# Optimization experiments

Measured on AMD Instinct MI355X. Metric: run time of the kernel, lower is better.

## Reference

```python
import jax, jax.numpy as jnp
import numpy as np

TEMPERATURE = 0.5


def setup_inputs() -> dict:
    key = jax.random.key(0)
    k1, k2 = jax.random.split(key)
    B, D = 4096, 256
    z_i = jax.random.normal(k1, (B, D), dtype=jnp.float32)
    z_j = jax.random.normal(k2, (B, D), dtype=jnp.float32)
    return {"z_i": z_i, "z_j": z_j}


def reference(z_i, z_j):
    B = z_i.shape[0]
    N = 2 * B
    z = jnp.concatenate([z_i, z_j], axis=0)                      # [N, D]
    # cosine similarity = normalized dot products (fused: normalize + matmul)
    zn = z / jnp.linalg.norm(z, axis=-1, keepdims=True)
    sim = jnp.einsum('nd,md->nm', zn, zn) / TEMPERATURE          # [N, N]
    # positives: sim[i, i+B] and sim[i+B, i]
    idx = jnp.arange(B)
    pos = jnp.concatenate([sim[idx, idx + B], sim[idx + B, idx]])  # [N]
    # cross-entropy with label 0 over logits [pos, negatives]:
    # logsumexp over row excluding only the diagonal (positive counted once)
    neg_inf = jnp.asarray(-jnp.inf, sim.dtype)
    sim_masked = jnp.where(jnp.eye(N, dtype=bool), neg_inf, sim)
    lse = jax.nn.logsumexp(sim_masked, axis=1)                    # [N]
    loss = jnp.sum(lse - pos) / N
    return loss
```

## Files before the change

kernel.cpp:

```cpp
#include <hip/hip_runtime.h>

typedef __attribute__((ext_vector_type(4))) float f32x4;
typedef __attribute__((ext_vector_type(2))) long long i64x2;

static constexpr int D = 256;
static constexpr float INV_T = 2.0f;
static constexpr float KEXP2 = 2.8853900817779268f;
static constexpr int TTILE = 64;
static constexpr int NT = TTILE * (TTILE + 1) / 2;
static constexpr int NPLANE = 2 * TTILE;
static constexpr int LSE_BLOCKS = 256;

__device__ inline float fexp2(float x) {
#if __has_builtin(__builtin_amdgcn_exp2f)
    return __builtin_amdgcn_exp2f(x);
#else
    return exp2f(x);
#endif
}
__device__ inline unsigned int cvt4_fp8(float a, float b, float c, float d) {
    int v = __builtin_amdgcn_cvt_pk_fp8_f32(a, b, 0, false);
    v = __builtin_amdgcn_cvt_pk_fp8_f32(c, d, v, true);
    return (unsigned int)v;
}

__global__ void k_norm(const float* __restrict__ zi, const float* __restrict__ zj,
                       unsigned char* __restrict__ zn, float* __restrict__ diag,
                       float* __restrict__ pos_partial, unsigned int* __restrict__ counter,
                       int B) {
    __shared__ float red[4];
    const int lane = threadIdx.x & 63;
    const int wv = threadIdx.x >> 6;
    const int i = blockIdx.x * 4 + wv;
    if (blockIdx.x == 0 && threadIdx.x == 0) *counter = 0;
    if (i < B) {
        float4 vi = reinterpret_cast<const float4*>(zi + (size_t)i * D)[lane];
        float4 vj = reinterpret_cast<const float4*>(zj + (size_t)i * D)[lane];
        float ssi = vi.x * vi.x + vi.y * vi.y + vi.z * vi.z + vi.w * vi.w;
        float ssj = vj.x * vj.x + vj.y * vj.y + vj.z * vj.z + vj.w * vj.w;
#pragma unroll
        for (int off = 32; off >= 1; off >>= 1) {
            ssi += __shfl_xor(ssi, off, 64);
            ssj += __shfl_xor(ssj, off, 64);
        }
        float rni = rsqrtf(ssi), rnj = rsqrtf(ssj);
        unsigned int pa = cvt4_fp8(vi.x * rni, vi.y * rni, vi.z * rni, vi.w * rni);
        unsigned int pb = cvt4_fp8(vj.x * rnj, vj.y * rnj, vj.z * rnj, vj.w * rnj);
        float fa0 = __builtin_amdgcn_cvt_f32_fp8((int)pa, 0);
        float fa1 = __builtin_amdgcn_cvt_f32_fp8((int)pa, 1);
        float fa2 = __builtin_amdgcn_cvt_f32_fp8((int)pa, 2);
        float fa3 = __builtin_amdgcn_cvt_f32_fp8((int)pa, 3);
        float fb0 = __builtin_amdgcn_cvt_f32_fp8((int)pb, 0);
        float fb1 = __builtin_amdgcn_cvt_f32_fp8((int)pb, 1);
        float fb2 = __builtin_amdgcn_cvt_f32_fp8((int)pb, 2);
        float fb3 = __builtin_amdgcn_cvt_f32_fp8((int)pb, 3);
        float sdi = fa0 * fa0 + fa1 * fa1 + fa2 * fa2 + fa3 * fa3;
        float sdj = fb0 * fb0 + fb1 * fb1 + fb2 * fb2 + fb3 * fb3;
        float pd  = fa0 * fb0 + fa1 * fb1 + fa2 * fb2 + fa3 * fb3;
#pragma unroll
        for (int off = 32; off >= 1; off >>= 1) {
            sdi += __shfl_xor(sdi, off, 64);
            sdj += __shfl_xor(sdj, off, 64);
            pd  += __shfl_xor(pd, off, 64);
        }
        unsigned int qa = __shfl_xor(pa, 1, 64);
        unsigned int qb = __shfl_xor(pb, 1, 64);
        if ((lane & 1) == 0) {
            int m = lane >> 1;
            size_t base = (size_t)(m >> 3) * 1024 + (size_t)((m & 3) * 16) * 16
                        + (size_t)(((m >> 2) & 1)) * 8;
            size_t offA = (size_t)(i >> 4) * 4096 + base + (size_t)(i & 15) * 16;
            int ib = i + B;
            size_t offB = (size_t)(ib >> 4) * 4096 + base + (size_t)(ib & 15) * 16;
            *reinterpret_cast<unsigned long long*>(zn + offA) =
                ((unsigned long long)qa << 32) | pa;
            *reinterpret_cast<unsigned long long*>(zn + offB) =
                ((unsigned long long)qb << 32) | pb;
        }
        if (lane == 0) {
            diag[i]     = -fexp2(KEXP2 * sdi);
            diag[i + B] = -fexp2(KEXP2 * sdj);
            red[wv] = pd;
        }
    } else if (lane == 0) {
        red[wv] = 0.f;
    }
    __syncthreads();
    if (threadIdx.x == 0)
        pos_partial[blockIdx.x] = 2.0f * INV_T * (red[0] + red[1] + red[2] + red[3]);
}

__global__ __launch_bounds__(128, 2)
void k_main(const unsigned char* __restrict__ zn, float* __restrict__ P, int N) {
    const int tid = threadIdx.x;
    const int lane = tid & 63;
    const int wc = tid >> 6;
    const int l15 = lane & 15, lhi = lane >> 4;

    const int bid = (int)blockIdx.x;
    const int swz = (bid & 7) * (NT / 8) + (bid >> 3);
    int ti = (int)(((float)(2 * TTILE + 1) -
                    sqrtf((float)((2 * TTILE + 1) * (2 * TTILE + 1)) - 8.0f * (float)swz)) * 0.5f);
    ti = (ti < 0) ? 0 : ((ti > TTILE - 1) ? TTILE - 1 : ti);
    while (ti > 0 && (ti * TTILE - ((ti * (ti - 1)) >> 1)) > swz) --ti;
    while (((ti + 1) * TTILE - (((ti + 1) * ti) >> 1)) <= swz) ++ti;
    const int tj = ti + (swz - (ti * TTILE - ((ti * (ti - 1)) >> 1)));

    const i64x2* Ap = reinterpret_cast<const i64x2*>(zn + (size_t)ti * 32768);
    const i64x2* Bp = reinterpret_cast<const i64x2*>(zn + (size_t)tj * 32768);

    f32x4 acc[8][4];
#pragma unroll
    for (int r = 0; r < 8; ++r)
#pragma unroll
        for (int c = 0; c < 4; ++c) acc[r][c] = (f32x4){0.f, 0.f, 0.f, 0.f};

#pragma unroll
    for (int kkp = 0; kkp < 4; ++kkp) {
        i64x2 a_[8], b_[4];
#pragma unroll
        for (int r = 0; r < 8; ++r)
            a_[r] = Ap[(r * 4 + kkp) * 64 + lane];
#pragma unroll
        for (int c = 0; c < 4; ++c)
            b_[c] = Bp[((wc * 4 + c) * 4 + kkp) * 64 + lane];
        __builtin_amdgcn_s_setprio(1);
#pragma unroll
        for (int r = 0; r < 8; ++r)
#pragma unroll
            for (int c = 0; c < 4; ++c)
                acc[r][c] = __builtin_amdgcn_mfma_f32_16x16x32_fp8_fp8(
                    a_[r].x, b_[c].x, acc[r][c], 0, 0, 0);
#pragma unroll
        for (int r = 0; r < 8; ++r)
#pragma unroll
            for (int c = 0; c < 4; ++c)
                acc[r][c] = __builtin_amdgcn_mfma_f32_16x16x32_fp8_fp8(
                    a_[r].y, b_[c].y, acc[r][c], 0, 0, 0);
        __builtin_amdgcn_s_setprio(0);
    }

    float cs[4] = {0.f, 0.f, 0.f, 0.f};
#pragma unroll
    for (int r = 0; r < 8; ++r) {
        float rq0 = 0.f, rq1 = 0.f, rq2 = 0.f, rq3 = 0.f;
#pragma unroll
        for (int c = 0; c < 4; ++c) {
            float e0 = fexp2(KEXP2 * acc[r][c][0]);
            float e1 = fexp2(KEXP2 * acc[r][c][1]);
            float e2 = fexp2(KEXP2 * acc[r][c][2]);
            float e3 = fexp2(KEXP2 * acc[r][c][3]);
            rq0 += e0; rq1 += e1; rq2 += e2; rq3 += e3;
            cs[c] += e0 + e1 + e2 + e3;
        }
#pragma unroll
        for (int off = 1; off <= 8; off <<= 1) {
            rq0 += __shfl_xor(rq0, off, 64);
            rq1 += __shfl_xor(rq1, off, 64);
            rq2 += __shfl_xor(rq2, off, 64);
            rq3 += __shfl_xor(rq3, off, 64);
        }
        if (l15 == 0) {
            f32x4 o = (f32x4){rq0, rq1, rq2, rq3};
            *reinterpret_cast<f32x4*>(
                P + (size_t)(2 * tj + wc) * N + ti * 128 + r * 16 + lhi * 4) = o;
        }
    }
    if (ti != tj) {
#pragma unroll
        for (int c = 0; c < 4; ++c) {
            float v = cs[c];
            v += __shfl_xor(v, 16, 64);
            v += __shfl_xor(v, 32, 64);
            if (lhi == 0)
                P[(size_t)(2 * ti + wc) * N + tj * 128 + wc * 64 + c * 16 + l15] = v;
        }
        P[(size_t)(2 * ti + wc) * N + tj * 128 + (1 - wc) * 64 + lane] = 0.f;
    }
}

__global__ void k_lse(const float* __restrict__ P, const float* __restrict__ diag,
                      const float* __restrict__ pos_partial, int n_pos,
                      float* __restrict__ part, unsigned int* __restrict__ counter,
                      float* __restrict__ out, int N) {
    __shared__ float red[4];
    const int tid = threadIdx.x;
    const int lane = tid & 63, wv = tid >> 6;
    const int row = blockIdx.x * 32 + (tid >> 3);
    const int sub = tid & 7;
    float s = 0.f;
#pragma unroll
    for (int d = 0; d < 16; ++d)
        s += P[(size_t)(sub * 16 + d) * N + row];
    s += __shfl_xor(s, 1, 64);
    s += __shfl_xor(s, 2, 64);
    s += __shfl_xor(s, 4, 64);
    float lg = (sub == 0) ? __logf(s + diag[row]) : 0.f;
    lg += __shfl_xor(lg, 8, 64);
    lg += __shfl_xor(lg, 16, 64);
    lg += __shfl_xor(lg, 32, 64);
    if (lane == 0) red[wv] = lg;
    __syncthreads();
    bool last = false;
    if (tid == 0) {
        part[blockIdx.x] = red[0] + red[1] + red[2] + red[3];
        __threadfence();
        last = (atomicAdd(counter, 1u) == LSE_BLOCKS - 1);
    }
    __shared__ int lastflag;
    if (tid == 0) lastflag = last ? 1 : 0;
    __syncthreads();
    if (lastflag) {
        __threadfence();
        float t = 0.f;
        for (int i = tid; i < LSE_BLOCKS; i += 256) t += part[i];
        for (int i = tid; i < n_pos; i += 256) t -= pos_partial[i];
#pragma unroll
        for (int off = 32; off >= 1; off >>= 1) t += __shfl_xor(t, off, 64);
        if (lane == 0) red[wv] = t;
        __syncthreads();
        if (tid == 0)
            out[0] = (red[0] + red[1] + red[2] + red[3]) / (float)N;
    }
}

extern "C" void kernel_launch(void* const* d_in, const int* in_sizes, int n_in,
                              void* d_out, int out_size, void* d_ws, size_t ws_size,
                              hipStream_t stream) {
    const float* zi = (const float*)d_in[0];
    const float* zj = (const float*)d_in[1];
    const int B = in_sizes[0] / D;
    const int N = 2 * B;

    char* ws = (char*)d_ws;
    unsigned char* zn = (unsigned char*)ws;
    float* diag = (float*)(ws + (size_t)N * D);
    float* pos_partial = diag + N;
    float* part = pos_partial + 1024;
    unsigned int* counter = (unsigned int*)(part + 256);
    float* P = (float*)(counter + 32);

    float* out = (float*)d_out;

    const int npb = B / 4;
    hipLaunchKernelGGL(k_norm, dim3(npb), dim3(256), 0, stream, zi, zj, zn, diag,
                       pos_partial, counter, B);
    hipLaunchKernelGGL(k_main, dim3(NT), dim3(128), 0, stream, zn, P, N);
    hipLaunchKernelGGL(k_lse, dim3(LSE_BLOCKS), dim3(256), 0, stream, P, diag,
                       pos_partial, npb, part, counter, out, N);
}
```

Before: 44.46 us.

## Switch FP8 GEMM to 32x32x64 scaled MFMA with matching operand layout

Replaces the 16x16x32 fp8 MFMA tiles with the gfx950 mfma_scale 32x32x64 f8f6f4 instruction using unit scales. The normalized fp8 operand layout written by k_norm is changed to match, with each lane now storing 32 contiguous bytes per K-chunk. The epilogue row and column reductions are reworked for the 32x32 accumulator layout. The aim is fewer MFMA issues and larger loads per lane, at the cost of more shuffle steps in the epilogue (5 per value instead of 4) and higher register pressure from the wider vectors.

```diff
diff --git a/kernel.cpp b/kernel.cpp
--- a/kernel.cpp
+++ b/kernel.cpp
@@ -1,7 +1,7 @@
 #include <hip/hip_runtime.h>
 
-typedef __attribute__((ext_vector_type(4))) float f32x4;
-typedef __attribute__((ext_vector_type(2))) long long i64x2;
+typedef __attribute__((ext_vector_type(16))) float f32x16;
+typedef __attribute__((ext_vector_type(8))) int i32x8;
 
 static constexpr int D = 256;
 static constexpr float INV_T = 2.0f;
@@ -10,6 +10,7 @@
 static constexpr int NT = TTILE * (TTILE + 1) / 2;
 static constexpr int NPLANE = 2 * TTILE;
 static constexpr int LSE_BLOCKS = 256;
+static constexpr unsigned int SCALE1 = 0x7F7F7F7Fu;
 
 __device__ inline float fexp2(float x) {
 #if __has_builtin(__builtin_amdgcn_exp2f)
@@ -22,6 +23,11 @@
     int v = __builtin_amdgcn_cvt_pk_fp8_f32(a, b, 0, false);
     v = __builtin_amdgcn_cvt_pk_fp8_f32(c, d, v, true);
     return (unsigned int)v;
+}
+__device__ inline size_t zoff(int row, int l) {
+    return (size_t)(row >> 7) * 32768 + (size_t)((row >> 5) & 3) * 8192
+         + (size_t)(l >> 4) * 2048 + (size_t)((l >> 3) & 1) * 1024
+         + (size_t)(row & 31) * 32 + (size_t)((l & 7) * 4);
 }
 
 __global__ void k_norm(const float* __restrict__ zi, const float* __restrict__ zj,
@@ -63,20 +69,8 @@
             sdj += __shfl_xor(sdj, off, 64);
             pd  += __shfl_xor(pd, off, 64);
         }
-        unsigned int qa = __shfl_xor(pa, 1, 64);
-        unsigned int qb = __shfl_xor(pb, 1, 64);
-        if ((lane & 1) == 0) {
-            int m = lane >> 1;
-            size_t base = (size_t)(m >> 3) * 1024 + (size_t)((m & 3) * 16) * 16
-                        + (size_t)(((m >> 2) & 1)) * 8;
-            size_t offA = (size_t)(i >> 4) * 4096 + base + (size_t)(i & 15) * 16;
-            int ib = i + B;
-            size_t offB = (size_t)(ib >> 4) * 4096 + base + (size_t)(ib & 15) * 16;
-            *reinterpret_cast<unsigned long long*>(zn + offA) =
-                ((unsigned long long)qa << 32) | pa;
-            *reinterpret_cast<unsigned long long*>(zn + offB) =
-                ((unsigned long long)qb << 32) | pb;
-        }
+        *reinterpret_cast<unsigned int*>(zn + zoff(i, lane)) = pa;
+        *reinterpret_cast<unsigned int*>(zn + zoff(i + B, lane)) = pb;
         if (lane == 0) {
             diag[i]     = -fexp2(KEXP2 * sdi);
             diag[i + B] = -fexp2(KEXP2 * sdj);
@@ -95,7 +89,7 @@
     const int tid = threadIdx.x;
     const int lane = tid & 63;
     const int wc = tid >> 6;
-    const int l15 = lane & 15, lhi = lane >> 4;
+    const int hi = lane >> 5;
 
     const int bid = (int)blockIdx.x;
     const int swz = (bid & 7) * (NT / 8) + (bid >> 3);
@@ -106,74 +100,70 @@
     while (((ti + 1) * TTILE - (((ti + 1) * ti) >> 1)) <= swz) ++ti;
     const int tj = ti + (swz - (ti * TTILE - ((ti * (ti - 1)) >> 1)));
 
-    const i64x2* Ap = reinterpret_cast<const i64x2*>(zn + (size_t)ti * 32768);
-    const i64x2* Bp = reinterpret_cast<const i64x2*>(zn + (size_t)tj * 32768);
-
-    f32x4 acc[8][4];
-#pragma unroll
-    for (int r = 0; r < 8; ++r)
-#pragma unroll
-        for (int c = 0; c < 4; ++c) acc[r][c] = (f32x4){0.f, 0.f, 0.f, 0.f};
-
-#pragma unroll
-    for (int kkp = 0; kkp < 4; ++kkp) {
-        i64x2 a_[8], b_[4];
-#pragma unroll
-        for (int r = 0; r < 8; ++r)
-            a_[r] = Ap[(r * 4 + kkp) * 64 + lane];
-#pragma unroll
-        for (int c = 0; c < 4; ++c)
-            b_[c] = Bp[((wc * 4 + c) * 4 + kkp) * 64 + lane];
+    const unsigned char* Abase = zn + (size_t)ti * 32768;
+    const unsigned char* Bbase = zn + (size_t)tj * 32768;
+
+    f32x16 acc[4][2];
+#pragma unroll
+    for (int rt = 0; rt < 4; ++rt)
+#pragma unroll
+        for (int ct = 0; ct < 2; ++ct)
+#pragma unroll
+            for (int g = 0; g < 16; ++g) acc[rt][ct][g] = 0.f;
+
+#pragma unroll
+    for (int kc = 0; kc < 4; ++kc) {
+        i32x8 a_[4], b_[2];
+#pragma unroll
+        for (int rt = 0; rt < 4; ++rt)
+            a_[rt] = *reinterpret_cast<const i32x8*>(Abase + (rt * 4 + kc) * 2048 + lane * 32);
+#pragma unroll
+        for (int ct = 0; ct < 2; ++ct)
+            b_[ct] = *reinterpret_cast<const i32x8*>(
+                Bbase + ((wc * 2 + ct) * 4 + kc) * 2048 + lane * 32);
         __builtin_amdgcn_s_setprio(1);
 #pragma unroll
-        for (int r = 0; r < 8; ++r)
-#pragma unroll
-            for (int c = 0; c < 4; ++c)
-                acc[r][c] = __builtin_amdgcn_mfma_f32_16x16x32_fp8_fp8(
-                    a_[r].x, b_[c].x, acc[r][c], 0, 0, 0);
-#pragma unroll
-        for (int r = 0; r < 8; ++r)
-#pragma unroll
-            for (int c = 0; c < 4; ++c)
-                acc[r][c] = __builtin_amdgcn_mfma_f32_16x16x32_fp8_fp8(
-                    a_[r].y, b_[c].y, acc[r][c], 0, 0, 0);
+        for (int rt = 0; rt < 4; ++rt)
+#pragma unroll
+            for (int ct = 0; ct < 2; ++ct)
+                acc[rt][ct] = __builtin_amdgcn_mfma_scale_f32_32x32x64_f8f6f4(
+                    a_[rt], b_[ct], acc[rt][ct], 0, 0, 0, SCALE1, 0, SCALE1);
         __builtin_amdgcn_s_setprio(0);
     }
 
-    float cs[4] = {0.f, 0.f, 0.f, 0.f};
-#pragma unroll
-    for (int r = 0; r < 8; ++r) {
-        float rq0 = 0.f, rq1 = 0.f, rq2 = 0.f, rq3 = 0.f;
-#pragma unroll
-        for (int c = 0; c < 4; ++c) {
-            float e0 = fexp2(KEXP2 * acc[r][c][0]);
-            float e1 = fexp2(KEXP2 * acc[r][c][1]);
-            float e2 = fexp2(KEXP2 * acc[r][c][2]);
-            float e3 = fexp2(KEXP2 * acc[r][c][3]);
-            rq0 += e0; rq1 += e1; rq2 += e2; rq3 += e3;
-            cs[c] += e0 + e1 + e2 + e3;
-        }
-#pragma unroll
-        for (int off = 1; off <= 8; off <<= 1) {
-            rq0 += __shfl_xor(rq0, off, 64);
-            rq1 += __shfl_xor(rq1, off, 64);
-            rq2 += __shfl_xor(rq2, off, 64);
-            rq3 += __shfl_xor(rq3, off, 64);
-        }
-        if (l15 == 0) {
-            f32x4 o = (f32x4){rq0, rq1, rq2, rq3};
-            *reinterpret_cast<f32x4*>(
-                P + (size_t)(2 * tj + wc) * N + ti * 128 + r * 16 + lhi * 4) = o;
+    float cs0 = 0.f, cs1 = 0.f;
+#pragma unroll
+    for (int rt = 0; rt < 4; ++rt) {
+        float rs[16];
+#pragma unroll
+        for (int g = 0; g < 16; ++g) {
+            float e0 = fexp2(KEXP2 * acc[rt][0][g]);
+            float e1 = fexp2(KEXP2 * acc[rt][1][g]);
+            rs[g] = e0 + e1;
+            cs0 += e0; cs1 += e1;
+        }
+#pragma unroll
+        for (int g = 0; g < 16; ++g) {
+            rs[g] += __shfl_xor(rs[g], 1, 64);
+            rs[g] += __shfl_xor(rs[g], 2, 64);
+            rs[g] += __shfl_xor(rs[g], 4, 64);
+            rs[g] += __shfl_xor(rs[g], 8, 64);
+            rs[g] += __shfl_xor(rs[g], 16, 64);
+        }
+        if ((lane & 31) == 0) {
+            float* Prow = P + (size_t)(2 * tj + wc) * N + ti * 128 + rt * 32 + 4 * hi;
+#pragma unroll
+            for (int g = 0; g < 16; ++g)
+                Prow[(g & 3) + 8 * (g >> 2)] = rs[g];
         }
     }
     if (ti != tj) {
-#pragma unroll
-        for (int c = 0; c < 4; ++c) {
-            float v = cs[c];
-            v += __shfl_xor(v, 16, 64);
-            v += __shfl_xor(v, 32, 64);
-            if (lhi == 0)
-                P[(size_t)(2 * ti + wc) * N + tj * 128 + wc * 64 + c * 16 + l15] = v;
+        cs0 += __shfl_xor(cs0, 32, 64);
+        cs1 += __shfl_xor(cs1, 32, 64);
+        float* Pcol = P + (size_t)(2 * ti + wc) * N + tj * 128 + wc * 64;
+        if (hi == 0) {
+            Pcol[lane] = cs0;
+            Pcol[32 + lane] = cs1;
         }
         P[(size_t)(2 * ti + wc) * N + tj * 128 + (1 - wc) * 64 + lane] = 0.f;
     }
```

After: 45.15 us. No clear change (+1.5%).
